# Optimization experiments

Hardware: AMD Instinct MI355X
Metric: run time of the kernel (lower is better)

Reference implementation:

```python
import jax, jax.numpy as jnp
import numpy as np

RADIUS = 0.5
K = 32  # num_neighbor


def ball_query(distances, radius, k):
    # distances: (B, M, N) squared distances; mark points outside radius with N,
    # then sort indices so in-range points (in original order) come first.
    B, M, N = distances.shape
    idx = jnp.where(distances >= radius ** 2, N,
                    jnp.arange(N, dtype=jnp.int32)[None, None, :])
    return jnp.sort(idx, axis=-1)[:, :, :k]  # (B, M, k), padded with N


def setup_inputs() -> dict:
    key = jax.random.key(0)
    ks = jax.random.split(key, 6)
    B, N, M, D, C = 4, 16384, 1024, 3, 64
    C_op, C_out = 64, 128
    positions = jax.random.normal(ks[0], (B, N, D), jnp.float32)
    features = jax.random.normal(ks[1], (B, N, C), jnp.float32)
    centers = jax.random.normal(ks[2], (B, M, D), jnp.float32)
    distances = jax.random.uniform(ks[3], (B, M, N), dtype=jnp.float32)
    W_op = jax.random.normal(ks[4], (D + C, C_op), jnp.float32) * 0.05
    b_op = jnp.zeros((C_op,), jnp.float32)
    W_agg = jax.random.normal(ks[5], (C_op, C_out), jnp.float32) * 0.05
    b_agg = jnp.zeros((C_out,), jnp.float32)
    return {"positions": positions, "features": features, "centers": centers,
            "distances": distances, "W_op": W_op, "b_op": b_op,
            "W_agg": W_agg, "b_agg": b_agg}


def reference(positions, features, centers, distances, W_op, b_op, W_agg, b_agg):
    B, N, D = positions.shape
    ids = ball_query(distances, RADIUS, K)      # (B, M, K); N marks invalid slot
    mask = ids != N                             # valid neighbor mask
    safe = jnp.where(mask, ids, 0)
    bidx = jnp.arange(B)[:, None, None]
    pos_n = positions[bidx, safe]               # (B, M, K, D) neighbor gather
    feat_n = features[bidx, safe]               # (B, M, K, C)
    rel = pos_n - centers[:, :, None, :]        # relative coordinates
    # NeighborOperator: pointwise linear on [rel_pos, features]
    f = jnp.concatenate([rel, feat_n], axis=-1) @ W_op + b_op  # (B, M, K, C_op)
    # invalid slots map to the zeros row in the torch index_put trick
    f = jnp.where(mask[..., None], f, 0.0)
    pooled = jnp.max(f, axis=2)                 # neighbor max-pool (B, M, C_op)
    # Conv1dBlock with kernel 1 == per-center linear + relu
    return jax.nn.relu(pooled @ W_agg + b_agg)  # (B, M, out_channels)
```

## Files before the change

### kernel.cpp

```cpp
#include <hip/hip_runtime.h>

constexpr int B_    = 4;
constexpr int N_    = 16384;
constexpr int M_    = 1024;
constexpr int C_    = 64;
constexpr int COP_  = 64;
constexpr int COUT_ = 128;
constexpr int K_    = 32;
constexpr float R2_ = 0.25f;

typedef __attribute__((ext_vector_type(8)))  short bf16x8;
typedef __attribute__((ext_vector_type(16))) float f32x16;

static __device__ __forceinline__ short f2bf(float f) {
    union { float f; unsigned u; } v; v.f = f;
    const unsigned r = v.u + 0x7fffu + ((v.u >> 16) & 1u);
    return (short)(r >> 16);
}

__global__ __launch_bounds__(64) void pointnet_fused(
    const float* __restrict__ positions,
    const float* __restrict__ features,
    const float* __restrict__ centers,
    const float* __restrict__ distances,
    const float* __restrict__ W_op,
    const float* __restrict__ b_op,
    const float* __restrict__ W_agg,
    const float* __restrict__ b_agg,
    float* __restrict__ out)
{
    const int lane = threadIdx.x;
    const int bm   = blockIdx.x;
    const int b    = bm >> 10;
    const int bN   = b * N_;

    __shared__ int s_ids[K_];
    if (lane < K_) s_ids[lane] = 0;

    const float* drow = distances + (size_t)bm * N_;
    float dch[4];
    #pragma unroll
    for (int i = 0; i < 4; ++i) dch[i] = drow[64 * i + lane];
    const unsigned long long ltmask = (1ull << lane) - 1ull;
    int found = 0;
    #pragma unroll
    for (int i = 0; i < 4; ++i) {
        const bool pred = dch[i] < R2_;
        const unsigned long long mi = __ballot(pred);
        const int rank = found + __popcll(mi & ltmask);
        if (pred && rank < K_) s_ids[rank] = 64 * i + lane;
        found += (int)__popcll(mi);
    }
    for (int n0 = 256; n0 < N_ && found < K_; n0 += 64) {
        const float d = drow[n0 + lane];
        const bool pred = d < R2_;
        const unsigned long long mi = __ballot(pred);
        const int rank = found + __popcll(mi & ltmask);
        if (pred && rank < K_) s_ids[rank] = n0 + lane;
        found += (int)__popcll(mi);
    }
    const int valid = found < K_ ? found : K_;

    const float ctr0 = centers[bm * 3 + 0];
    const float ctr1 = centers[bm * 3 + 1];
    const float ctr2 = centers[bm * 3 + 2];

    const int rowid = s_ids[lane & (K_ - 1)];
    const int koff  = (lane >> 5) * 8;

    const float* frow = features + (size_t)(bN + rowid) * C_;
    float4 xa[8];
    #pragma unroll
    for (int s = 0; s < 4; ++s) {
        xa[2 * s]     = *(const float4*)(frow + 16 * s + koff);
        xa[2 * s + 1] = *(const float4*)(frow + 16 * s + koff + 4);
    }
    const float* prow = positions + (size_t)(bN + rowid) * 3;
    const float r0 = prow[0] - ctr0;
    const float r1 = prow[1] - ctr1;
    const float r2 = prow[2] - ctr2;

    bf16x8 afr[5];
    #pragma unroll
    for (int s = 0; s < 4; ++s) {
        afr[s][0] = f2bf(xa[2 * s].x);     afr[s][1] = f2bf(xa[2 * s].y);
        afr[s][2] = f2bf(xa[2 * s].z);     afr[s][3] = f2bf(xa[2 * s].w);
        afr[s][4] = f2bf(xa[2 * s + 1].x); afr[s][5] = f2bf(xa[2 * s + 1].y);
        afr[s][6] = f2bf(xa[2 * s + 1].z); afr[s][7] = f2bf(xa[2 * s + 1].w);
    }
    #pragma unroll
    for (int j = 0; j < 8; ++j) afr[4][j] = 0;
    if (koff == 0) { afr[4][0] = f2bf(r0); afr[4][1] = f2bf(r1); afr[4][2] = f2bf(r2); }

    const int n0col = lane & 31;
    bf16x8 bfr[2][5];
    #pragma unroll
    for (int t = 0; t < 2; ++t) {
        const int n = 32 * t + n0col;
        #pragma unroll
        for (int s = 0; s < 4; ++s)
            #pragma unroll
            for (int j = 0; j < 8; ++j)
                bfr[t][s][j] = f2bf(W_op[(3 + 16 * s + koff + j) * COP_ + n]);
        #pragma unroll
        for (int j = 0; j < 8; ++j) {
            const int c = koff + j;
            bfr[t][4][j] = (c < 3) ? f2bf(W_op[c * COP_ + n]) : (short)0;
        }
    }

    f32x16 acc0, acc1;
    #pragma unroll
    for (int i = 0; i < 16; ++i) { acc0[i] = 0.0f; acc1[i] = 0.0f; }
    #pragma unroll
    for (int s = 0; s < 5; ++s) {
        acc0 = __builtin_amdgcn_mfma_f32_32x32x16_bf16(afr[s], bfr[0][s], acc0, 0, 0, 0);
        acc1 = __builtin_amdgcn_mfma_f32_32x32x16_bf16(afr[s], bfr[1][s], acc1, 0, 0, 0);
    }

    const float bb0 = b_op[n0col];
    const float bb1 = b_op[32 + n0col];
    const int mbase = 4 * (lane >> 5);
    float p0 = -INFINITY, p1 = -INFINITY;
    #pragma unroll
    for (int r = 0; r < 16; ++r) {
        const int m = (r & 3) + 8 * (r >> 2) + mbase;
        const bool ok = m < valid;
        p0 = fmaxf(p0, ok ? (acc0[r] + bb0) : 0.0f);
        p1 = fmaxf(p1, ok ? (acc1[r] + bb1) : 0.0f);
    }
    p0 = fmaxf(p0, __shfl_xor(p0, 32));
    p1 = fmaxf(p1, __shfl_xor(p1, 32));

    float a0 = b_agg[lane];
    float a1 = b_agg[lane + 64];
    #pragma unroll
    for (int jj = 0; jj < 32; ++jj) {
        const float q0 = __int_as_float(__builtin_amdgcn_readlane(__float_as_int(p0), jj));
        a0 = fmaf(q0, W_agg[jj * COUT_ + lane],      a0);
        a1 = fmaf(q0, W_agg[jj * COUT_ + lane + 64], a1);
        const float q1 = __int_as_float(__builtin_amdgcn_readlane(__float_as_int(p1), jj));
        a0 = fmaf(q1, W_agg[(32 + jj) * COUT_ + lane],      a0);
        a1 = fmaf(q1, W_agg[(32 + jj) * COUT_ + lane + 64], a1);
    }
    float* orow = out + (size_t)bm * COUT_;
    orow[lane]      = fmaxf(a0, 0.0f);
    orow[lane + 64] = fmaxf(a1, 0.0f);
}

extern "C" void kernel_launch(void* const* d_in, const int* in_sizes, int n_in,
                              void* d_out, int out_size, void* d_ws, size_t ws_size,
                              hipStream_t stream) {
    const float* positions = (const float*)d_in[0];
    const float* features  = (const float*)d_in[1];
    const float* centers   = (const float*)d_in[2];
    const float* distances = (const float*)d_in[3];
    const float* W_op      = (const float*)d_in[4];
    const float* b_op      = (const float*)d_in[5];
    const float* W_agg     = (const float*)d_in[6];
    const float* b_agg     = (const float*)d_in[7];
    float* out = (float*)d_out;

    dim3 grid(B_ * M_);
    dim3 block(64);
    pointnet_fused<<<grid, block, 0, stream>>>(
        positions, features, centers, distances,
        W_op, b_op, W_agg, b_agg, out);
}
```

Measured before the change: 326.6 us.

## Split each center's output channels across two wavefronts per block

Each block now runs two wavefronts instead of one. Both repeat the ball query scan. Each wave then computes half of the C_op columns with MFMA, and the pooled values are exchanged through shared memory so each wave can produce half of the output channels. This halves the per-wave MFMA, weight-conversion and aggregation work and lowers register pressure. The cost is a duplicated distance scan, duplicated feature loads and an added block barrier.

Measured after the change: 328.5 us. No clear change (+0.6%).

```diff
diff --git a/kernel.cpp b/kernel.cpp
--- a/kernel.cpp
+++ b/kernel.cpp
@@ -18,7 +18,7 @@
     return (short)(r >> 16);
 }
 
-__global__ __launch_bounds__(64) void pointnet_fused(
+__global__ __launch_bounds__(128) void pointnet_fused(
     const float* __restrict__ positions,
     const float* __restrict__ features,
     const float* __restrict__ centers,
@@ -29,13 +29,15 @@
     const float* __restrict__ b_agg,
     float* __restrict__ out)
 {
-    const int lane = threadIdx.x;
+    const int lane = threadIdx.x & 63;
+    const int wv   = threadIdx.x >> 6;
     const int bm   = blockIdx.x;
     const int b    = bm >> 10;
     const int bN   = b * N_;
 
-    __shared__ int s_ids[K_];
-    if (lane < K_) s_ids[lane] = 0;
+    __shared__ int   s_ids[2][K_];
+    __shared__ float s_pool[COP_];
+    if (lane < K_) s_ids[wv][lane] = 0;
 
     const float* drow = distances + (size_t)bm * N_;
     float dch[4];
@@ -48,7 +50,7 @@
         const bool pred = dch[i] < R2_;
         const unsigned long long mi = __ballot(pred);
         const int rank = found + __popcll(mi & ltmask);
-        if (pred && rank < K_) s_ids[rank] = 64 * i + lane;
+        if (pred && rank < K_) s_ids[wv][rank] = 64 * i + lane;
         found += (int)__popcll(mi);
     }
     for (int n0 = 256; n0 < N_ && found < K_; n0 += 64) {
@@ -56,7 +58,7 @@
         const bool pred = d < R2_;
         const unsigned long long mi = __ballot(pred);
         const int rank = found + __popcll(mi & ltmask);
-        if (pred && rank < K_) s_ids[rank] = n0 + lane;
+        if (pred && rank < K_) s_ids[wv][rank] = n0 + lane;
         found += (int)__popcll(mi);
     }
     const int valid = found < K_ ? found : K_;
@@ -65,7 +67,7 @@
     const float ctr1 = centers[bm * 3 + 1];
     const float ctr2 = centers[bm * 3 + 2];
 
-    const int rowid = s_ids[lane & (K_ - 1)];
+    const int rowid = s_ids[wv][lane & (K_ - 1)];
     const int koff  = (lane >> 5) * 8;
 
     const float* frow = features + (size_t)(bN + rowid) * C_;
@@ -93,59 +95,48 @@
     if (koff == 0) { afr[4][0] = f2bf(r0); afr[4][1] = f2bf(r1); afr[4][2] = f2bf(r2); }
 
     const int n0col = lane & 31;
-    bf16x8 bfr[2][5];
+    const int ncol  = 32 * wv + n0col;
+    bf16x8 bfr[5];
     #pragma unroll
-    for (int t = 0; t < 2; ++t) {
-        const int n = 32 * t + n0col;
+    for (int s = 0; s < 4; ++s)
         #pragma unroll
-        for (int s = 0; s < 4; ++s)
-            #pragma unroll
-            for (int j = 0; j < 8; ++j)
-                bfr[t][s][j] = f2bf(W_op[(3 + 16 * s + koff + j) * COP_ + n]);
-        #pragma unroll
-        for (int j = 0; j < 8; ++j) {
-            const int c = koff + j;
-            bfr[t][4][j] = (c < 3) ? f2bf(W_op[c * COP_ + n]) : (short)0;
-        }
+        for (int j = 0; j < 8; ++j)
+            bfr[s][j] = f2bf(W_op[(3 + 16 * s + koff + j) * COP_ + ncol]);
+    #pragma unroll
+    for (int j = 0; j < 8; ++j) {
+        const int c = koff + j;
+        bfr[4][j] = (c < 3) ? f2bf(W_op[c * COP_ + ncol]) : (short)0;
     }
 
-    f32x16 acc0, acc1;
+    f32x16 acc;
     #pragma unroll
-    for (int i = 0; i < 16; ++i) { acc0[i] = 0.0f; acc1[i] = 0.0f; }
+    for (int i = 0; i < 16; ++i) acc[i] = 0.0f;
     #pragma unroll
-    for (int s = 0; s < 5; ++s) {
-        acc0 = __builtin_amdgcn_mfma_f32_32x32x16_bf16(afr[s], bfr[0][s], acc0, 0, 0, 0);
-        acc1 = __builtin_amdgcn_mfma_f32_32x32x16_bf16(afr[s], bfr[1][s], acc1, 0, 0, 0);
-    }
+    for (int s = 0; s < 5; ++s)
+        acc = __builtin_amdgcn_mfma_f32_32x32x16_bf16(afr[s], bfr[s], acc, 0, 0, 0);
 
-    const float bb0 = b_op[n0col];
-    const float bb1 = b_op[32 + n0col];
+    const float bb = b_op[ncol];
     const int mbase = 4 * (lane >> 5);
-    float p0 = -INFINITY, p1 = -INFINITY;
+    float p = -INFINITY;
     #pragma unroll
     for (int r = 0; r < 16; ++r) {
         const int m = (r & 3) + 8 * (r >> 2) + mbase;
-        const bool ok = m < valid;
-        p0 = fmaxf(p0, ok ? (acc0[r] + bb0) : 0.0f);
-        p1 = fmaxf(p1, ok ? (acc1[r] + bb1) : 0.0f);
+        p = fmaxf(p, (m < valid) ? (acc[r] + bb) : 0.0f);
     }
-    p0 = fmaxf(p0, __shfl_xor(p0, 32));
-    p1 = fmaxf(p1, __shfl_xor(p1, 32));
+    p = fmaxf(p, __shfl_xor(p, 32));
 
-    float a0 = b_agg[lane];
-    float a1 = b_agg[lane + 64];
+    if (lane < 32) s_pool[ncol] = p;
+    __syncthreads();
+    const float pfull = s_pool[lane];
+
+    float a = b_agg[64 * wv + lane];
     #pragma unroll
-    for (int jj = 0; jj < 32; ++jj) {
-        const float q0 = __int_as_float(__builtin_amdgcn_readlane(__float_as_int(p0), jj));
-        a0 = fmaf(q0, W_agg[jj * COUT_ + lane],      a0);
-        a1 = fmaf(q0, W_agg[jj * COUT_ + lane + 64], a1);
-        const float q1 = __int_as_float(__builtin_amdgcn_readlane(__float_as_int(p1), jj));
-        a0 = fmaf(q1, W_agg[(32 + jj) * COUT_ + lane],      a0);
-        a1 = fmaf(q1, W_agg[(32 + jj) * COUT_ + lane + 64], a1);
+    for (int jj = 0; jj < COP_; ++jj) {
+        const float q = __int_as_float(
+            __builtin_amdgcn_readlane(__float_as_int(pfull), jj));
+        a = fmaf(q, W_agg[jj * COUT_ + 64 * wv + lane], a);
     }
-    float* orow = out + (size_t)bm * COUT_;
-    orow[lane]      = fmaxf(a0, 0.0f);
-    orow[lane + 64] = fmaxf(a1, 0.0f);
+    out[(size_t)bm * COUT_ + 64 * wv + lane] = fmaxf(a, 0.0f);
 }
 
 extern "C" void kernel_launch(void* const* d_in, const int* in_sizes, int n_in,
@@ -162,7 +153,7 @@
     float* out = (float*)d_out;
 
     dim3 grid(B_ * M_);
-    dim3 block(64);
+    dim3 block(128);
     pointnet_fused<<<grid, block, 0, stream>>>(
         positions, features, centers, distances,
         W_op, b_op, W_agg, b_agg, out);
```
